# Kernel optimization log

Hardware: AMD Instinct MI355X
Metric: run time of the kernel (lower is better)

Reference implementation:

```python
import jax, jax.numpy as jnp
import numpy as np

B, L, D = 64, 4096, 256

def setup_inputs() -> dict:
    key = jax.random.key(0)
    k1, k2 = jax.random.split(key)
    inp = jax.random.normal(k1, (B, L, D), dtype=jnp.float32)
    # lengths in [1, L] so no empty-sequence mean (matches original assumption)
    length = jax.random.randint(k2, (B,), 1, L + 1, dtype=jnp.int64)
    return {"input": inp, "length": length}

def reference(input, length):
    # One fused masked mean over the ragged sequence dim.
    # mask: [B, L] True for valid positions
    mask = (jnp.arange(input.shape[1])[None, :] < length[:, None])
    m = mask.astype(input.dtype)[:, :, None]            # [B, L, 1]
    summed = jnp.sum(input * m, axis=1)                  # [B, D]
    return summed / length.astype(input.dtype)[:, None] # [B, D]
```

## Files before the change

### kernel.cpp

```cpp
#include <hip/hip_runtime.h>

#define BB 64
#define LL 4096
#define DD 256
#define PP 64
#define ROWS_PER_CHUNK (LL / PP)
#define D4 (DD / 4)
#define WAVES 4

__global__ __launch_bounds__(256) void avg_partial_kernel(
    const float* __restrict__ in,
    const int* __restrict__ len,
    float* __restrict__ ws)
{
    const int w    = threadIdx.x >> 6;
    const int lane = threadIdx.x & 63;
    const int c    = blockIdx.x * WAVES + w;
    const int b    = c >> 6;
    const int p    = c & 63;

    const int lb      = len[b];
    const int nchunks = (lb + ROWS_PER_CHUNK - 1) >> 6;
    if (p >= nchunks) return;

    const int row0 = p * ROWS_PER_CHUNK;
    int rend = row0 + ROWS_PER_CHUNK;
    if (rend > lb) rend = lb;

    float4 acc = make_float4(0.f, 0.f, 0.f, 0.f);
    const float4* __restrict__ base = (const float4*)(in + (size_t)b * LL * DD);

    #pragma unroll 8
    for (int r = row0; r < rend; ++r) {
        float4 v = base[(size_t)r * D4 + lane];
        acc.x += v.x; acc.y += v.y; acc.z += v.z; acc.w += v.w;
    }

    float4* __restrict__ wsb = (float4*)ws + ((size_t)b * PP + p) * D4;
    wsb[lane] = acc;
}

__global__ __launch_bounds__(256) void avg_reduce_kernel(
    const float* __restrict__ ws,
    const int* __restrict__ len,
    float* __restrict__ out)
{
    const int b    = blockIdx.x;
    const int w    = threadIdx.x >> 6;
    const int lane = threadIdx.x & 63;

    int lb = len[b];
    if (lb < 1) lb = 1;
    const int nchunks = (lb + ROWS_PER_CHUNK - 1) >> 6;

    float4 acc = make_float4(0.f, 0.f, 0.f, 0.f);
    const float4* __restrict__ wsb = (const float4*)ws + (size_t)b * PP * D4;

    for (int p = w; p < nchunks; p += WAVES) {
        float4 v = wsb[(size_t)p * D4 + lane];
        acc.x += v.x; acc.y += v.y; acc.z += v.z; acc.w += v.w;
    }

    __shared__ float4 sh[WAVES - 1][64];
    if (w > 0) sh[w - 1][lane] = acc;
    __syncthreads();

    if (w == 0) {
        #pragma unroll
        for (int i = 0; i < WAVES - 1; ++i) {
            float4 v = sh[i][lane];
            acc.x += v.x; acc.y += v.y; acc.z += v.z; acc.w += v.w;
        }
        const float inv = 1.0f / (float)lb;
        float4 o = make_float4(acc.x * inv, acc.y * inv, acc.z * inv, acc.w * inv);
        ((float4*)out)[(size_t)b * D4 + lane] = o;
    }
}

__global__ void avg_zero_out_kernel(float* __restrict__ out) {
    int i = blockIdx.x * blockDim.x + threadIdx.x;
    if (i < BB * DD) out[i] = 0.f;
}

__global__ __launch_bounds__(64) void avg_atomic_kernel(
    const float* __restrict__ in,
    const int* __restrict__ len,
    float* __restrict__ out)
{
    const int b    = blockIdx.x / PP;
    const int p    = blockIdx.x % PP;
    const int lane = threadIdx.x;

    int lb = len[b];
    if (lb < 1) lb = 1;
    const int row0 = p * ROWS_PER_CHUNK;
    int rend = row0 + ROWS_PER_CHUNK;
    if (rend > lb) rend = (lb > row0) ? lb : row0;
    if (rend <= row0) return;

    float4 acc = make_float4(0.f, 0.f, 0.f, 0.f);
    const float4* __restrict__ base = (const float4*)(in + (size_t)b * LL * DD);
    for (int r = row0; r < rend; ++r) {
        float4 v = base[(size_t)r * D4 + lane];
        acc.x += v.x; acc.y += v.y; acc.z += v.z; acc.w += v.w;
    }
    const float inv = 1.0f / (float)lb;
    float* o = out + (size_t)b * DD + lane * 4;
    atomicAdd(o + 0, acc.x * inv);
    atomicAdd(o + 1, acc.y * inv);
    atomicAdd(o + 2, acc.z * inv);
    atomicAdd(o + 3, acc.w * inv);
}

extern "C" void kernel_launch(void* const* d_in, const int* in_sizes, int n_in,
                              void* d_out, int out_size, void* d_ws, size_t ws_size,
                              hipStream_t stream) {
    const float* in  = (const float*)d_in[0];
    const int*   len = (const int*)d_in[1];
    float*       out = (float*)d_out;

    const size_t ws_needed = (size_t)BB * PP * DD * sizeof(float);

    if (ws_size >= ws_needed && d_ws != nullptr) {
        float* ws = (float*)d_ws;
        avg_partial_kernel<<<(BB * PP) / WAVES, 256, 0, stream>>>(in, len, ws);
        avg_reduce_kernel<<<BB, 256, 0, stream>>>(ws, len, out);
    } else {
        avg_zero_out_kernel<<<(BB * DD + 255) / 256, 256, 0, stream>>>(out);
        avg_atomic_kernel<<<BB * PP, 64, 0, stream>>>(in, len, out);
    }
}
```

Measured before the change: 33.79 us.

## Interleave batch across waves, unroll full chunks, widen reduce block

Work is now mapped batch-fastest, so consecutive waves and blocks handle different batches instead of clustering all chunks of one sequence. This spreads ragged-length imbalance across CUs and avoids whole blocks exiting early. Full chunks take a fully unrolled path that issues eight independent loads at once and accumulates into two partial sums to increase memory-level parallelism. The reduce kernel uses 8 waves per block instead of 4, shortening each wave's serial accumulation.

```diff
diff --git a/kernel.cpp b/kernel.cpp
--- a/kernel.cpp
+++ b/kernel.cpp
@@ -7,6 +7,7 @@
 #define ROWS_PER_CHUNK (LL / PP)
 #define D4 (DD / 4)
 #define WAVES 4
+#define RWAVES 8
 
 __global__ __launch_bounds__(256) void avg_partial_kernel(
     const float* __restrict__ in,
@@ -16,31 +17,51 @@
     const int w    = threadIdx.x >> 6;
     const int lane = threadIdx.x & 63;
     const int c    = blockIdx.x * WAVES + w;
-    const int b    = c >> 6;
-    const int p    = c & 63;
+    const int b    = c & (BB - 1);
+    const int p    = c >> 6;
 
-    const int lb      = len[b];
-    const int nchunks = (lb + ROWS_PER_CHUNK - 1) >> 6;
-    if (p >= nchunks) return;
+    const int lb   = len[b];
+    const int row0 = p << 6;
+    if (row0 >= lb) return;
 
-    const int row0 = p * ROWS_PER_CHUNK;
-    int rend = row0 + ROWS_PER_CHUNK;
-    if (rend > lb) rend = lb;
+    const float4* __restrict__ base =
+        (const float4*)(in + (size_t)b * LL * DD) + (size_t)row0 * D4 + lane;
 
-    float4 acc = make_float4(0.f, 0.f, 0.f, 0.f);
-    const float4* __restrict__ base = (const float4*)(in + (size_t)b * LL * DD);
+    int n = lb - row0;
+    if (n > ROWS_PER_CHUNK) n = ROWS_PER_CHUNK;
 
-    #pragma unroll 8
-    for (int r = row0; r < rend; ++r) {
-        float4 v = base[(size_t)r * D4 + lane];
-        acc.x += v.x; acc.y += v.y; acc.z += v.z; acc.w += v.w;
+    float4 a0 = make_float4(0.f, 0.f, 0.f, 0.f);
+    float4 a1 = make_float4(0.f, 0.f, 0.f, 0.f);
+
+    if (n == ROWS_PER_CHUNK) {
+        #pragma unroll
+        for (int r = 0; r < ROWS_PER_CHUNK; r += 8) {
+            float4 v0 = base[(size_t)(r + 0) * D4];
+            float4 v1 = base[(size_t)(r + 1) * D4];
+            float4 v2 = base[(size_t)(r + 2) * D4];
+            float4 v3 = base[(size_t)(r + 3) * D4];
+            float4 v4 = base[(size_t)(r + 4) * D4];
+            float4 v5 = base[(size_t)(r + 5) * D4];
+            float4 v6 = base[(size_t)(r + 6) * D4];
+            float4 v7 = base[(size_t)(r + 7) * D4];
+            a0.x += v0.x + v2.x + v4.x + v6.x;  a1.x += v1.x + v3.x + v5.x + v7.x;
+            a0.y += v0.y + v2.y + v4.y + v6.y;  a1.y += v1.y + v3.y + v5.y + v7.y;
+            a0.z += v0.z + v2.z + v4.z + v6.z;  a1.z += v1.z + v3.z + v5.z + v7.z;
+            a0.w += v0.w + v2.w + v4.w + v6.w;  a1.w += v1.w + v3.w + v5.w + v7.w;
+        }
+    } else {
+        for (int r = 0; r < n; ++r) {
+            float4 v = base[(size_t)r * D4];
+            a0.x += v.x; a0.y += v.y; a0.z += v.z; a0.w += v.w;
+        }
     }
 
+    float4 acc = make_float4(a0.x + a1.x, a0.y + a1.y, a0.z + a1.z, a0.w + a1.w);
     float4* __restrict__ wsb = (float4*)ws + ((size_t)b * PP + p) * D4;
     wsb[lane] = acc;
 }
 
-__global__ __launch_bounds__(256) void avg_reduce_kernel(
+__global__ __launch_bounds__(512) void avg_reduce_kernel(
     const float* __restrict__ ws,
     const int* __restrict__ len,
     float* __restrict__ out)
@@ -56,18 +77,19 @@
     float4 acc = make_float4(0.f, 0.f, 0.f, 0.f);
     const float4* __restrict__ wsb = (const float4*)ws + (size_t)b * PP * D4;
 
-    for (int p = w; p < nchunks; p += WAVES) {
+    #pragma unroll 2
+    for (int p = w; p < nchunks; p += RWAVES) {
         float4 v = wsb[(size_t)p * D4 + lane];
         acc.x += v.x; acc.y += v.y; acc.z += v.z; acc.w += v.w;
     }
 
-    __shared__ float4 sh[WAVES - 1][64];
+    __shared__ float4 sh[RWAVES - 1][64];
     if (w > 0) sh[w - 1][lane] = acc;
     __syncthreads();
 
     if (w == 0) {
         #pragma unroll
-        for (int i = 0; i < WAVES - 1; ++i) {
+        for (int i = 0; i < RWAVES - 1; ++i) {
             float4 v = sh[i][lane];
             acc.x += v.x; acc.y += v.y; acc.z += v.z; acc.w += v.w;
         }
@@ -124,7 +146,7 @@
     if (ws_size >= ws_needed && d_ws != nullptr) {
         float* ws = (float*)d_ws;
         avg_partial_kernel<<<(BB * PP) / WAVES, 256, 0, stream>>>(in, len, ws);
-        avg_reduce_kernel<<<BB, 256, 0, stream>>>(ws, len, out);
+        avg_reduce_kernel<<<BB, 512, 0, stream>>>(ws, len, out);
     } else {
         avg_zero_out_kernel<<<(BB * DD + 255) / 256, 256, 0, stream>>>(out);
         avg_atomic_kernel<<<BB * PP, 64, 0, stream>>>(in, len, out);
```

Result: slower. 39.84 us (+17.9%).
